# Performance work log

Measured on AMD Instinct MI355X. Metric: run time of the kernel, lower is better.

Reference implementation:

```python
import jax, jax.numpy as jnp
import numpy as np

STRIDES = (8, 16, 32, 64)
NUM_HEADS = 8
G = 4
P = 32
TAU_Z = 2.0
LVL_BASE = 3.0  # stride 8 == 2**3 maps to level 0


def decode_box(xyzr):
    scale = jnp.exp2(xyzr[..., 2:3])
    ratio = jnp.exp2(jnp.concatenate([-0.5 * xyzr[..., 3:4], 0.5 * xyzr[..., 3:4]], axis=-1))
    wh = scale * ratio
    xy = xyzr[..., 0:2]
    return jnp.concatenate([xy - 0.5 * wh, xy + 0.5 * wh], axis=-1)


def position_embedding(box, num_feats, temperature=10000.0):
    term = jnp.array([1000.0, 1000.0, 1.0, 1.0], dtype=box.dtype)
    token = box / term
    dim_t = jnp.arange(num_feats, dtype=jnp.float32)
    dim_t = temperature ** (2.0 * (dim_t // 2) / num_feats)
    pos = token[..., None] / dim_t  # B,N,4,F
    pos = jnp.stack([jnp.sin(pos[..., 0::2]), jnp.cos(pos[..., 1::2])], axis=4)
    B, N = box.shape[:2]
    return pos.reshape(B, N, -1)  # B,N,4*F


def bbox_iof(boxes):
    # boxes: B,N,4 x1y1x2y2; iof[b,i,j] = inter(i,j) / area(i)
    area = jnp.clip(boxes[..., 2] - boxes[..., 0], 0.0) * jnp.clip(boxes[..., 3] - boxes[..., 1], 0.0)
    lt = jnp.maximum(boxes[:, :, None, :2], boxes[:, None, :, :2])
    rb = jnp.minimum(boxes[:, :, None, 2:], boxes[:, None, :, 2:])
    wh = jnp.clip(rb - lt, 0.0)
    inter = wh[..., 0] * wh[..., 1]
    return inter / jnp.clip(area[:, :, None], 1e-7, None)


def bilinear_group_sample(feat, xy, stride):
    # feat: [B,C,H,W]; xy: [B,N,P,G,2] image coords -> [B,N,G,P,C//G]
    B, C, H, W = feat.shape
    _, N, Pn, Gn, _ = xy.shape
    Cg = C // Gn
    featg = feat.reshape(B, Gn, Cg, H * W).transpose(0, 1, 3, 2)  # B,G,HW,Cg
    px = xy[..., 0] / stride - 0.5  # grid_sample align_corners=False convention
    py = xy[..., 1] / stride - 0.5
    x0 = jnp.floor(px)
    y0 = jnp.floor(py)
    bi = jnp.arange(B)[:, None, None]
    gi = jnp.arange(Gn)[None, :, None]
    out = jnp.zeros((B, Gn, N * Pn, Cg), dtype=feat.dtype)
    for dx in (0.0, 1.0):
        for dy in (0.0, 1.0):
            xi = x0 + dx
            yi = y0 + dy
            wgt = (1.0 - jnp.abs(px - xi)) * (1.0 - jnp.abs(py - yi))
            valid = (xi >= 0) & (xi <= W - 1) & (yi >= 0) & (yi <= H - 1)
            wgt = wgt * valid  # zero padding outside
            xi_c = jnp.clip(xi, 0, W - 1).astype(jnp.int32)
            yi_c = jnp.clip(yi, 0, H - 1).astype(jnp.int32)
            idx = (yi_c * W + xi_c).transpose(0, 3, 1, 2).reshape(B, Gn, N * Pn)
            vals = featg[bi, gi, idx]  # B,G,N*P,Cg
            w = wgt.transpose(0, 3, 1, 2).reshape(B, Gn, N * Pn, 1)
            out = out + vals * w
    return out.reshape(B, Gn, N, Pn, Cg).transpose(0, 2, 1, 3, 4)


def layer_norm(x, g, b, eps=1e-5):
    mu = jnp.mean(x, axis=-1, keepdims=True)
    var = jnp.mean((x - mu) ** 2, axis=-1, keepdims=True)
    return (x - mu) * jax.lax.rsqrt(var + eps) * g + b


def _forward(feats, query_content, query_box, Wq, bq, Wk, bk, Wv, bv, Wo, bo,
             ln_g, ln_b, off_W, off_b, sc_W, sc_b, iof_tau):
    B, N, C = query_content.shape
    H = NUM_HEADS
    dh = C // H
    box_cxcy = query_box[..., :2]
    zc = query_box[..., 2:3]
    rc = query_box[..., 3:4]
    box_wh = jnp.exp2(zc) * jnp.exp2(jnp.concatenate([-0.5 * rc, 0.5 * rc], axis=-1))
    logscale = zc.reshape(B, N, 1, 1)

    # torch.no_grad() block -> stop_gradient
    rois = decode_box(query_box)
    iof = jnp.log(bbox_iof(jax.lax.stop_gradient(rois)) + 1e-7)  # B,N,N
    pe = jax.lax.stop_gradient(position_embedding(query_box, C // 4))  # B,N,C
    attn_bias = iof[:, None, :, :] * iof_tau.reshape(1, -1, 1, 1)  # B,H,N,N

    x = query_content + pe
    q = (x @ Wq.T + bq).reshape(B, N, H, dh)
    k = (x @ Wk.T + bk).reshape(B, N, H, dh)
    v = (x @ Wv.T + bv).reshape(B, N, H, dh)
    scores = jnp.einsum('bnhd,bmhd->bhnm', q, k) * (dh ** -0.5) + attn_bias
    attn = jax.nn.softmax(scores, axis=-1)
    ctx = jnp.einsum('bhnm,bmhd->bnhd', attn, v).reshape(B, N, C)
    qc = x + ctx @ Wo.T + bo  # mmcv MultiheadAttention adds identity (= query+pe)
    qc = layer_norm(qc, ln_g, ln_b)

    offset = (qc @ off_W.T + off_b).reshape(B, N, P, G, 2)
    scale_logit = (qc @ sc_W.T + sc_b).reshape(B, N, P, G)
    sample_xy = box_cxcy.reshape(B, N, 1, 1, 2) + offset * box_wh.reshape(B, N, 1, 1, 2)
    sample_z = scale_logit + logscale  # B,N,P,G
    lvl = sample_z - LVL_BASE
    levels = jnp.arange(len(STRIDES), dtype=jnp.float32)
    zw = jax.nn.softmax(-((lvl[..., None] - levels) ** 2) / TAU_Z, axis=-1)  # B,N,P,G,L
    zw_t = zw.transpose(0, 1, 3, 2, 4)  # B,N,G,P,L
    sample_feats = jnp.zeros(())
    for l, (fm, s) in enumerate(zip(feats, STRIDES)):
        sample_feats = sample_feats + bilinear_group_sample(fm, sample_xy, s) * zw_t[..., l:l + 1]
    return sample_feats, sample_xy, offset, sample_z, scale_logit, qc


def setup_inputs():
    key = jax.random.key(0)
    ks = jax.random.split(key, 20)
    B, N, C = 4, 500, 256
    feat0 = jax.random.normal(ks[0], (B, C, 128, 128), dtype=jnp.float32)
    feat1 = jax.random.normal(ks[1], (B, C, 64, 64), dtype=jnp.float32)
    feat2 = jax.random.normal(ks[2], (B, C, 32, 32), dtype=jnp.float32)
    feat3 = jax.random.normal(ks[3], (B, C, 16, 16), dtype=jnp.float32)
    query_content = jax.random.normal(ks[4], (B, N, C), dtype=jnp.float32)
    xy = jax.random.uniform(ks[5], (B, N, 2), minval=64.0, maxval=960.0)
    zz = jax.random.uniform(ks[6], (B, N, 1), minval=3.0, maxval=6.0)
    rr = jax.random.uniform(ks[7], (B, N, 1), minval=-1.0, maxval=1.0)
    query_box = jnp.concatenate([xy, zz, rr], axis=-1)
    sub_query_xy = jax.random.normal(ks[8], (B, N, P, G, 2), dtype=jnp.float32) * 0.1
    sub_query_z = jax.random.normal(ks[9], (B, N, P, G, 4), dtype=jnp.float32) * 0.1
    sub_query_vec = jax.random.normal(ks[10], (B, N, P, G, 64), dtype=jnp.float32) * 0.1
    imgs_whwh = jnp.full((B, N, 4), 1024.0, dtype=jnp.float32)
    w = lambda i, sh: jax.random.normal(ks[i], sh, dtype=jnp.float32) * 0.02
    return {
        'feat0': feat0, 'feat1': feat1, 'feat2': feat2, 'feat3': feat3,
        'query_content': query_content, 'query_box': query_box,
        'sub_query_xy': sub_query_xy, 'sub_query_z': sub_query_z,
        'sub_query_vec': sub_query_vec, 'imgs_whwh': imgs_whwh,
        'Wq': w(11, (C, C)), 'bq': jnp.zeros((C,), jnp.float32),
        'Wk': w(12, (C, C)), 'bk': jnp.zeros((C,), jnp.float32),
        'Wv': w(13, (C, C)), 'bv': jnp.zeros((C,), jnp.float32),
        'Wo': w(14, (C, C)), 'bo': jnp.zeros((C,), jnp.float32),
        'ln_g': jnp.ones((C,), jnp.float32), 'ln_b': jnp.zeros((C,), jnp.float32),
        'off_W': w(15, (2 * G * P, C)),
        'off_b': jax.random.uniform(ks[16], (2 * G * P,), minval=-0.5, maxval=0.5),
        'sc_W': w(17, (G * P, C)),
        'sc_b': jax.random.normal(ks[18], (G * P,), dtype=jnp.float32) * 0.1,
        'iof_tau': jax.random.uniform(ks[19], (NUM_HEADS,), minval=0.0, maxval=4.0),
    }


def reference(feat0, feat1, feat2, feat3, query_content, query_box, sub_query_xy,
              sub_query_z, sub_query_vec, imgs_whwh, Wq, bq, Wk, bk, Wv, bv, Wo, bo,
              ln_g, ln_b, off_W, off_b, sc_W, sc_b, iof_tau):
    sample_feats, sample_xy, offset, sample_z, scale_logit, qc = _forward(
        [feat0, feat1, feat2, feat3], query_content, query_box,
        Wq, bq, Wk, bk, Wv, bv, Wo, bo, ln_g, ln_b, off_W, off_b, sc_W, sc_b, iof_tau)
    return (sample_feats, sub_query_xy, sub_query_z, sub_query_vec, qc,
            sample_xy, offset, sample_z, scale_logit)
```

## Files before the change

### kernel.cpp

```cpp
#include <hip/hip_runtime.h>
#include <cstdint>
#include <cstddef>

#define B_ 4
#define N_ 500
#define C_ 256
#define NH_ 8
#define DH_ 32
#define P_ 32
#define G_ 4
#define CG_ 64
#define BN_ (B_*N_)

__constant__ const int LVL_W[4] = {128, 64, 32, 16};

static __device__ __forceinline__ unsigned short f2bf(float f) {
  union { float f; unsigned u; } v; v.f = f;
  unsigned r = v.u + 0x7FFF + ((v.u >> 16) & 1);
  return (unsigned short)(r >> 16);
}
static __device__ __forceinline__ float bf2f(unsigned u16shifted) {
  union { unsigned u; float f; } v; v.u = u16shifted;
  return v.f;
}

__global__ __launch_bounds__(256) void mega_kernel(
    const float* __restrict__ f0, const float* __restrict__ f1,
    const float* __restrict__ f2, const float* __restrict__ f3,
    unsigned short* __restrict__ t0, unsigned short* __restrict__ t1,
    unsigned short* __restrict__ t2, unsigned short* __restrict__ t3,
    const float* __restrict__ subxy, const float* __restrict__ subz,
    const float* __restrict__ subv,
    float* __restrict__ o_subxy, float* __restrict__ o_subz,
    float* __restrict__ o_subv, int tblocks) {
  __shared__ float tile[64][65];
  int blk = blockIdx.x;
  int t = threadIdx.x;
  if (blk < tblocks) {
    const float* src; unsigned short* dst; int npix, i;
    if (blk < 4096)      { src = f0; dst = t0; npix = 16384; i = blk; }
    else if (blk < 5120) { src = f1; dst = t1; npix = 4096;  i = blk - 4096; }
    else if (blk < 5376) { src = f2; dst = t2; npix = 1024;  i = blk - 5120; }
    else                 { src = f3; dst = t3; npix = 256;   i = blk - 5376; }
    int pb = npix >> 6;
    int p0 = (i % pb) * 64;
    int c0 = ((i / pb) & 3) * 64;
    int b  = i / (pb * 4);
    for (int k = 0; k < 16; k++) {
      int cl = k * 4 + (t >> 6);
      int pl = t & 63;
      tile[cl][pl] = src[((size_t)b * C_ + (c0 + cl)) * npix + (p0 + pl)];
    }
    __syncthreads();
    int cq = t & 15;
    for (int k = 0; k < 4; k++) {
      int pl = k * 16 + (t >> 4);
      ushort4 r;
      r.x = f2bf(tile[cq * 4 + 0][pl]);
      r.y = f2bf(tile[cq * 4 + 1][pl]);
      r.z = f2bf(tile[cq * 4 + 2][pl]);
      r.w = f2bf(tile[cq * 4 + 3][pl]);
      *(ushort4*)&dst[((size_t)b * npix + (p0 + pl)) * C_ + c0 + cq * 4] = r;
    }
  } else {
    int cb = blk - tblocks;
    const float4* s4; float4* d4;
    if (cb < 125)      { s4 = (const float4*)subxy + (size_t)cb * 1024;
                         d4 = (float4*)o_subxy + (size_t)cb * 1024; }
    else if (cb < 375) { s4 = (const float4*)subz + (size_t)(cb - 125) * 1024;
                         d4 = (float4*)o_subz + (size_t)(cb - 125) * 1024; }
    else               { s4 = (const float4*)subv + (size_t)(cb - 375) * 1024;
                         d4 = (float4*)o_subv + (size_t)(cb - 375) * 1024; }
    d4[t] = s4[t];
    d4[t + 256] = s4[t + 256];
    d4[t + 512] = s4[t + 512];
    d4[t + 768] = s4[t + 768];
  }
}

#define QKV_QI 8
__global__ __launch_bounds__(256) void qkv_prep_kernel(
    const float* __restrict__ qcontent, const float* __restrict__ qbox,
    const float* __restrict__ Wq, const float* __restrict__ bq,
    const float* __restrict__ Wk, const float* __restrict__ bk,
    const float* __restrict__ Wv, const float* __restrict__ bv,
    float* __restrict__ x, float* __restrict__ boxd,
    float* __restrict__ q, float* __restrict__ kT, float* __restrict__ vT) {
  __shared__ float xs[QKV_QI][C_];
  int blk = blockIdx.x;
  int t = threadIdx.x;
  int bn0 = blk * QKV_QI;
  int d = t >> 6;
  float tj = exp2f((float)((t >> 1) & 31) * 0.4152410f);
  float tmul = (d < 2) ? 0.001f : 1.0f;
  for (int i = 0; i < QKV_QI; i++) {
    float qv = qbox[(size_t)(bn0 + i) * 4 + d];
    float val = qv * tmul / tj;
    float pe = (t & 1) ? cosf(val) : sinf(val);
    float xv = qcontent[(size_t)(bn0 + i) * C_ + t] + pe;
    xs[i][t] = xv;
    x[(size_t)(bn0 + i) * C_ + t] = xv;
  }
  if (t < QKV_QI) {
    int bn = bn0 + t;
    const float* qb = qbox + (size_t)bn * 4;
    float cx = qb[0], cy = qb[1], z = qb[2], r = qb[3];
    float scale = exp2f(z);
    float w = scale * exp2f(-0.5f * r);
    float h = scale * exp2f(0.5f * r);
    float* bd = boxd + (size_t)bn * 12;
    float x1 = cx - 0.5f * w, y1 = cy - 0.5f * h, x2 = cx + 0.5f * w, y2 = cy + 0.5f * h;
    bd[0] = x1; bd[1] = y1; bd[2] = x2; bd[3] = y2;
    bd[4] = cx; bd[5] = cy; bd[6] = w; bd[7] = h; bd[8] = z;
    float area = fmaxf(x2 - x1, 0.f) * fmaxf(y2 - y1, 0.f);
    bd[9] = fmaxf(area, 1e-7f);
  }
  __syncthreads();
  float accq[QKV_QI], acck[QKV_QI], accv[QKV_QI];
  for (int i = 0; i < QKV_QI; i++) { accq[i] = 0.f; acck[i] = 0.f; accv[i] = 0.f; }
  const float4* wq4 = (const float4*)(Wq + (size_t)t * C_);
  const float4* wk4 = (const float4*)(Wk + (size_t)t * C_);
  const float4* wv4 = (const float4*)(Wv + (size_t)t * C_);
  for (int k4 = 0; k4 < C_ / 4; k4++) {
    float4 wq = wq4[k4], wk = wk4[k4], wv = wv4[k4];
    for (int i = 0; i < QKV_QI; i++) {
      float4 xv = *(const float4*)&xs[i][k4 * 4];
      accq[i] += xv.x * wq.x + xv.y * wq.y + xv.z * wq.z + xv.w * wq.w;
      acck[i] += xv.x * wk.x + xv.y * wk.y + xv.z * wk.z + xv.w * wk.w;
      accv[i] += xv.x * wv.x + xv.y * wv.y + xv.z * wv.z + xv.w * wv.w;
    }
  }
  for (int i = 0; i < QKV_QI; i++) {
    int bn = bn0 + i;
    int b = bn / N_;
    int n = bn % N_;
    q[(size_t)bn * C_ + t] = accq[i] + bq[t];
    kT[((size_t)b * C_ + t) * N_ + n] = acck[i] + bk[t];
    vT[((size_t)b * C_ + t) * N_ + n] = accv[i] + bv[t];
  }
}

__global__ __launch_bounds__(256) void score_kernel(
    const float* __restrict__ q, const float* __restrict__ kT,
    const float* __restrict__ boxd, const float* __restrict__ tau_p,
    float* __restrict__ S, float* __restrict__ Mpart) {
  int mp = blockIdx.x >> 1;
  int npar = blockIdx.x & 1;
  int h = blockIdx.y;
  int b = blockIdx.z;
  int w = threadIdx.x >> 6;
  int lane = threadIdx.x & 63;
  int m = mp * 64 + lane;
  int mc = min(m, N_ - 1);
  bool mok = m < N_;
  float tau = tau_p[h];
  const float scl = 0.17677669529663687f;

  float kreg[DH_];
  const float* kbase = kT + ((size_t)b * C_ + h * DH_) * N_ + mc;
#pragma unroll
  for (int d = 0; d < DH_; d++) kreg[d] = kbase[(size_t)d * N_];

  const float* bm = boxd + ((size_t)b * N_ + mc) * 12;
  float kx1 = bm[0], ky1 = bm[1], kx2 = bm[2], ky2 = bm[3];

  size_t srow_base = ((size_t)(b * NH_ + h)) * N_;
  for (int n = npar * 4 + w; n < N_; n += 8) {
    const float* qn = q + ((size_t)b * N_ + n) * C_ + h * DH_;
    float4 q0 = *(const float4*)&qn[0];
    float4 q1 = *(const float4*)&qn[4];
    float4 q2 = *(const float4*)&qn[8];
    float4 q3 = *(const float4*)&qn[12];
    float4 q4 = *(const float4*)&qn[16];
    float4 q5 = *(const float4*)&qn[20];
    float4 q6 = *(const float4*)&qn[24];
    float4 q7 = *(const float4*)&qn[28];
    float s0 = q0.x*kreg[0] + q0.y*kreg[1] + q0.z*kreg[2] + q0.w*kreg[3];
    float s1 = q1.x*kreg[4] + q1.y*kreg[5] + q1.z*kreg[6] + q1.w*kreg[7];
    float s2 = q2.x*kreg[8] + q2.y*kreg[9] + q2.z*kreg[10] + q2.w*kreg[11];
    float s3 = q3.x*kreg[12] + q3.y*kreg[13] + q3.z*kreg[14] + q3.w*kreg[15];
    s0 += q4.x*kreg[16] + q4.y*kreg[17] + q4.z*kreg[18] + q4.w*kreg[19];
    s1 += q5.x*kreg[20] + q5.y*kreg[21] + q5.z*kreg[22] + q5.w*kreg[23];
    s2 += q6.x*kreg[24] + q6.y*kreg[25] + q6.z*kreg[26] + q6.w*kreg[27];
    s3 += q7.x*kreg[28] + q7.y*kreg[29] + q7.z*kreg[30] + q7.w*kreg[31];
    float s = (s0 + s1) + (s2 + s3);

    const float* bn = boxd + ((size_t)b * N_ + n) * 12;
    float4 nb = *(const float4*)&bn[0];
    float inv_area = 1.0f / bn[9];
    float iw = fmaxf(fminf(nb.z, kx2) - fmaxf(nb.x, kx1), 0.f);
    float ih = fmaxf(fminf(nb.w, ky2) - fmaxf(nb.y, ky1), 0.f);
    float bias = logf(iw * ih * inv_area + 1e-7f);
    float sc = s * scl + bias * tau;

    if (mok) S[(srow_base + n) * 512 + m] = sc;
    float wm = mok ? sc : -1e30f;
#pragma unroll
    for (int off = 32; off >= 1; off >>= 1) wm = fmaxf(wm, __shfl_xor(wm, off, 64));
    if (lane == 0) Mpart[(srow_base + n) * 8 + mp] = wm;
  }
}

__global__ __launch_bounds__(256) void pv_kernel(
    const float* __restrict__ S, const float* __restrict__ Mpart,
    const float* __restrict__ vT, float* __restrict__ ctx) {
  int w = threadIdx.x >> 6;
  int lane = threadIdx.x & 63;
  int n0 = blockIdx.x * 4;
  int h = blockIdx.y * 4 + w;
  int b = blockIdx.z;
  size_t rb = ((size_t)(b * NH_ + h)) * N_;

  float mval = -1e30f;
  if (lane < 32) mval = Mpart[(rb + n0 + (lane >> 3)) * 8 + (lane & 7)];
  mval = fmaxf(mval, __shfl_xor(mval, 1, 64));
  mval = fmaxf(mval, __shfl_xor(mval, 2, 64));
  mval = fmaxf(mval, __shfl_xor(mval, 4, 64));
  float mx[4];
#pragma unroll
  for (int n = 0; n < 4; n++) mx[n] = __shfl(mval, n * 8, 64);

  float p[4][8];
  float inv[4];
#pragma unroll
  for (int n = 0; n < 4; n++) {
    const float* Srow = S + (rb + n0 + n) * 512;
    float sum = 0.f;
#pragma unroll
    for (int i = 0; i < 8; i++) {
      int m = lane + 64 * i;
      float sv = Srow[min(m, N_ - 1)];
      float e = (m < N_) ? __expf(sv - mx[n]) : 0.f;
      p[n][i] = e;
      sum += e;
    }
#pragma unroll
    for (int off = 32; off >= 1; off >>= 1) sum += __shfl_xor(sum, off, 64);
    inv[n] = 1.0f / sum;
  }

  const float* vbase = vT + ((size_t)b * C_ + h * DH_) * N_;
  float keep0 = 0.f, keep1 = 0.f, keep2 = 0.f, keep3 = 0.f;
  for (int cc = 0; cc < DH_; cc++) {
    const float* vrow = vbase + (size_t)cc * N_;
    float a0 = 0.f, a1 = 0.f, a2 = 0.f, a3 = 0.f;
#pragma unroll
    for (int i = 0; i < 8; i++) {
      int m = lane + 64 * i;
      float vv = vrow[min(m, N_ - 1)];
      a0 += p[0][i] * vv;
      a1 += p[1][i] * vv;
      a2 += p[2][i] * vv;
      a3 += p[3][i] * vv;
    }
#pragma unroll
    for (int off = 32; off >= 1; off >>= 1) {
      a0 += __shfl_xor(a0, off, 64);
      a1 += __shfl_xor(a1, off, 64);
      a2 += __shfl_xor(a2, off, 64);
      a3 += __shfl_xor(a3, off, 64);
    }
    bool sel = (lane & 31) == cc;
    keep0 = sel ? a0 : keep0;
    keep1 = sel ? a1 : keep1;
    keep2 = sel ? a2 : keep2;
    keep3 = sel ? a3 : keep3;
  }
  int c = lane & 31;
  size_t obase = ((size_t)b * N_ + n0) * C_ + h * DH_ + c;
  if (lane < 32) {
    ctx[obase + 0 * C_] = keep0 * inv[0];
    ctx[obase + 2 * C_] = keep2 * inv[2];
  } else {
    ctx[obase + 1 * C_] = keep1 * inv[1];
    ctx[obase + 3 * C_] = keep3 * inv[3];
  }
}

#define PQI 4
__global__ __launch_bounds__(256) void projln_head_kernel(
    const float* __restrict__ ctx, const float* __restrict__ x,
    const float* __restrict__ Wo, const float* __restrict__ bo,
    const float* __restrict__ ln_g, const float* __restrict__ ln_b,
    const float* __restrict__ boxd,
    const float* __restrict__ offW, const float* __restrict__ offb,
    const float* __restrict__ scW, const float* __restrict__ scb,
    float* __restrict__ qc_out,
    float* __restrict__ out_offset, float* __restrict__ out_sxy,
    float* __restrict__ out_sz, float* __restrict__ out_sl,
    float* __restrict__ zw_ws) {
  __shared__ float cs[PQI][C_];
  __shared__ float qs[PQI][C_];
  __shared__ float redbuf[PQI][8];
  int blk = blockIdx.x;
  int t = threadIdx.x;
  int bn0 = blk * PQI;
  for (int i = 0; i < PQI; i++) cs[i][t] = ctx[(size_t)(bn0 + i) * C_ + t];
  __syncthreads();
  float acc[PQI] = {0.f, 0.f, 0.f, 0.f};
  {
    const float4* w4 = (const float4*)(Wo + (size_t)t * C_);
    for (int k4 = 0; k4 < C_ / 4; k4++) {
      float4 w = w4[k4];
      for (int i = 0; i < PQI; i++) {
        float4 cv = *(const float4*)&cs[i][k4 * 4];
        acc[i] += cv.x * w.x + cv.y * w.y + cv.z * w.z + cv.w * w.w;
      }
    }
  }
  float y[PQI];
  int wave = t >> 6, lane = t & 63;
  for (int i = 0; i < PQI; i++) {
    y[i] = x[(size_t)(bn0 + i) * C_ + t] + acc[i] + bo[t];
    float s1 = y[i], s2 = y[i] * y[i];
#pragma unroll
    for (int off = 32; off >= 1; off >>= 1) {
      s1 += __shfl_xor(s1, off, 64);
      s2 += __shfl_xor(s2, off, 64);
    }
    if (lane == 0) { redbuf[i][wave] = s1; redbuf[i][wave + 4] = s2; }
  }
  __syncthreads();
  for (int i = 0; i < PQI; i++) {
    float s1 = redbuf[i][0] + redbuf[i][1] + redbuf[i][2] + redbuf[i][3];
    float s2 = redbuf[i][4] + redbuf[i][5] + redbuf[i][6] + redbuf[i][7];
    float mu = s1 * (1.0f / C_);
    float var = s2 * (1.0f / C_) - mu * mu;
    float inv = rsqrtf(var + 1e-5f);
    float o = (y[i] - mu) * inv * ln_g[t] + ln_b[t];
    qs[i][t] = o;
    qc_out[(size_t)(bn0 + i) * C_ + t] = o;
  }
  __syncthreads();
  float ao[PQI] = {0.f, 0.f, 0.f, 0.f};
  {
    const float4* w4 = (const float4*)(offW + (size_t)t * C_);
    for (int k4 = 0; k4 < C_ / 4; k4++) {
      float4 w = w4[k4];
      for (int i = 0; i < PQI; i++) {
        float4 cv = *(const float4*)&qs[i][k4 * 4];
        ao[i] += cv.x * w.x + cv.y * w.y + cv.z * w.z + cv.w * w.w;
      }
    }
  }
  int xy = t & 1;
  for (int i = 0; i < PQI; i++) {
    int bn = bn0 + i;
    const float* bd = boxd + (size_t)bn * 12;
    float off = ao[i] + offb[t];
    float ctr = xy ? bd[5] : bd[4];
    float wh = xy ? bd[7] : bd[6];
    float sxy = ctr + off * wh;
    out_offset[(size_t)bn * 256 + t] = off;
    out_sxy[(size_t)bn * 256 + t] = sxy;
  }
  if (t < 128) {
    float as[PQI] = {0.f, 0.f, 0.f, 0.f};
    const float4* sw4 = (const float4*)(scW + (size_t)t * C_);
    for (int k4 = 0; k4 < C_ / 4; k4++) {
      float4 w = sw4[k4];
      for (int i = 0; i < PQI; i++) {
        float4 cv = *(const float4*)&qs[i][k4 * 4];
        as[i] += cv.x * w.x + cv.y * w.y + cv.z * w.z + cv.w * w.w;
      }
    }
    for (int i = 0; i < PQI; i++) {
      int bn = bn0 + i;
      const float* bd = boxd + (size_t)bn * 12;
      float sl = as[i] + scb[t];
      float sz = sl + bd[8];
      out_sl[(size_t)bn * 128 + t] = sl;
      out_sz[(size_t)bn * 128 + t] = sz;
      float lvl = sz - 3.0f;
      float d1 = lvl - 1.f, d2 = lvl - 2.f, d3 = lvl - 3.f;
      float e0 = __expf(-0.5f * lvl * lvl);
      float e1 = __expf(-0.5f * d1 * d1);
      float e2 = __expf(-0.5f * d2 * d2);
      float e3 = __expf(-0.5f * d3 * d3);
      float inv = 1.0f / (e0 + e1 + e2 + e3);
      float* zw = zw_ws + ((size_t)bn * 128 + t) * 4;
      zw[0] = e0 * inv; zw[1] = e1 * inv; zw[2] = e2 * inv; zw[3] = e3 * inv;
    }
  }
}

__global__ __launch_bounds__(256) void sample_kernel_v3(
    const unsigned short* __restrict__ f0, const unsigned short* __restrict__ f1,
    const unsigned short* __restrict__ f2, const unsigned short* __restrict__ f3,
    const float* __restrict__ sxy, const float* __restrict__ zw_ws,
    float* __restrict__ out) {
  int t = threadIdx.x;
  int wv = t >> 6;
  int lane = t & 63;
  int sub = lane >> 4;
  int c4 = lane & 15;
  int pt = blockIdx.x * 16 + wv * 4 + sub;
  int g = pt & 3;
  int p = (pt >> 2) & 31;
  int bn = pt >> 7;
  int b = bn / N_;

  float sx = sxy[(size_t)pt * 2];
  float sy = sxy[(size_t)pt * 2 + 1];
  const float* zw = zw_ws + (size_t)pt * 4;
  const unsigned short* feats[4] = {f0, f1, f2, f3};
  const float inv_stride[4] = {0.125f, 0.0625f, 0.03125f, 0.015625f};
  float4 acc = {0.f, 0.f, 0.f, 0.f};
#pragma unroll
  for (int l = 0; l < 4; l++) {
    float wl = zw[l];
    int W = LVL_W[l];
    float px = sx * inv_stride[l] - 0.5f;
    float py = sy * inv_stride[l] - 0.5f;
    float x0f = floorf(px), y0f = floorf(py);
    float fx = px - x0f, fy = py - y0f;
    int x0 = (int)x0f, y0 = (int)y0f;
    const unsigned short* fb = feats[l] + (size_t)b * W * W * C_ + g * CG_ + c4 * 4;
#pragma unroll
    for (int dy = 0; dy < 2; dy++) {
#pragma unroll
      for (int dx = 0; dx < 2; dx++) {
        int xi = x0 + dx, yi = y0 + dy;
        float valid = (xi >= 0 && xi < W && yi >= 0 && yi < W) ? 1.f : 0.f;
        int xc = min(max(xi, 0), W - 1);
        int yc = min(max(yi, 0), W - 1);
        float wgt = (dx ? fx : 1.f - fx) * (dy ? fy : 1.f - fy) * valid * wl;
        uint2 u = *(const uint2*)&fb[((size_t)yc * W + xc) * C_];
        acc.x += wgt * bf2f(u.x << 16);
        acc.y += wgt * bf2f(u.x & 0xFFFF0000u);
        acc.z += wgt * bf2f(u.y << 16);
        acc.w += wgt * bf2f(u.y & 0xFFFF0000u);
      }
    }
  }
  *(float4*)&out[(size_t)bn * 8192 + g * 2048 + p * 64 + c4 * 4] = acc;
}

__global__ __launch_bounds__(256) void sample_kernel_native(
    const float* __restrict__ f0, const float* __restrict__ f1,
    const float* __restrict__ f2, const float* __restrict__ f3,
    const float* __restrict__ sxy, const float* __restrict__ zw_ws,
    float* __restrict__ out) {
  int t = threadIdx.x;
  int wv = t >> 6;
  int lane = t & 63;
  int pt = blockIdx.x * 4 + wv;
  int g = pt & 3;
  int p = (pt >> 2) & 31;
  int bn = pt >> 7;
  int b = bn / N_;
  float sx = sxy[(size_t)pt * 2];
  float sy = sxy[(size_t)pt * 2 + 1];
  const float* zw = zw_ws + (size_t)pt * 4;
  const float* feats[4] = {f0, f1, f2, f3};
  const float inv_stride[4] = {0.125f, 0.0625f, 0.03125f, 0.015625f};
  float acc = 0.f;
#pragma unroll
  for (int l = 0; l < 4; l++) {
    float wl = zw[l];
    int W = LVL_W[l];
    float px = sx * inv_stride[l] - 0.5f;
    float py = sy * inv_stride[l] - 0.5f;
    float x0f = floorf(px), y0f = floorf(py);
    float fx = px - x0f, fy = py - y0f;
    int x0 = (int)x0f, y0 = (int)y0f;
#pragma unroll
    for (int dy = 0; dy < 2; dy++) {
#pragma unroll
      for (int dx = 0; dx < 2; dx++) {
        int xi = x0 + dx, yi = y0 + dy;
        if (xi >= 0 && xi < W && yi >= 0 && yi < W) {
          float wgt = (dx ? fx : 1.f - fx) * (dy ? fy : 1.f - fy);
          float v = feats[l][(((size_t)b * C_ + g * CG_ + lane) * W + yi) * W + xi];
          acc += wgt * wl * v;
        }
      }
    }
  }
  out[(size_t)bn * 8192 + g * 2048 + p * 64 + lane] = acc;
}

extern "C" void kernel_launch(void* const* d_in, const int* in_sizes, int n_in,
                              void* d_out, int out_size, void* d_ws, size_t ws_size,
                              hipStream_t stream) {
  (void)in_sizes; (void)n_in; (void)out_size;
  const float* feat[4] = {(const float*)d_in[0], (const float*)d_in[1],
                          (const float*)d_in[2], (const float*)d_in[3]};
  const float* query_content = (const float*)d_in[4];
  const float* query_box = (const float*)d_in[5];
  const float* Wq = (const float*)d_in[10]; const float* bq = (const float*)d_in[11];
  const float* Wk = (const float*)d_in[12]; const float* bk = (const float*)d_in[13];
  const float* Wv = (const float*)d_in[14]; const float* bv = (const float*)d_in[15];
  const float* Wo = (const float*)d_in[16]; const float* bo = (const float*)d_in[17];
  const float* ln_g = (const float*)d_in[18]; const float* ln_b = (const float*)d_in[19];
  const float* offW = (const float*)d_in[20]; const float* offb = (const float*)d_in[21];
  const float* scW = (const float*)d_in[22]; const float* scb = (const float*)d_in[23];
  const float* iof_tau = (const float*)d_in[24];

  float* out = (float*)d_out;
  float* ws = (float*)d_ws;

  const size_t O_FEATS = 0;
  const size_t O_SUBXY = 16384000;
  const size_t O_SUBZ = 16896000;
  const size_t O_SUBV = 17920000;
  const size_t O_QC = 34304000;
  const size_t O_SXY = 34816000;
  const size_t O_OFF = 35328000;
  const size_t O_SZ = 35840000;
  const size_t O_SL = 36096000;

  float* S = out + O_FEATS;
  float* Mpart = out + O_FEATS + 8192000;

  const size_t o_x = 0;
  const size_t o_boxd = o_x + 512000;
  const size_t o_q = o_boxd + 24000;
  const size_t o_kT = o_q + 512000;
  const size_t o_vT = o_kT + 512000;
  const size_t o_ctx = o_vT + 512000;
  const size_t o_zw = o_ctx + 512000;
  const size_t o_ft = o_zw + 1024000;
  const size_t ft_sz[4] = {16777216, 4194304, 1048576, 262144};
  const size_t ft_total = ft_sz[0] + ft_sz[1] + ft_sz[2] + ft_sz[3];
  const size_t need_T = o_ft * sizeof(float) + ft_total * sizeof(unsigned short);
  const bool useT = ws_size >= need_T;

  unsigned short* ftu = (unsigned short*)(ws + o_ft);
  unsigned short* ftb[4] = {ftu,
                            ftu + ft_sz[0],
                            ftu + ft_sz[0] + ft_sz[1],
                            ftu + ft_sz[0] + ft_sz[1] + ft_sz[2]};

  const int tblocks = useT ? 5440 : 0;
  const int cblocks = 4375;
  mega_kernel<<<tblocks + cblocks, 256, 0, stream>>>(
      feat[0], feat[1], feat[2], feat[3],
      ftb[0], ftb[1], ftb[2], ftb[3],
      (const float*)d_in[6], (const float*)d_in[7], (const float*)d_in[8],
      out + O_SUBXY, out + O_SUBZ, out + O_SUBV, tblocks);

  qkv_prep_kernel<<<BN_ / QKV_QI, 256, 0, stream>>>(
      query_content, query_box, Wq, bq, Wk, bk, Wv, bv,
      ws + o_x, ws + o_boxd, ws + o_q, ws + o_kT, ws + o_vT);

  {
    dim3 ga(16, NH_, B_);
    score_kernel<<<ga, 256, 0, stream>>>(ws + o_q, ws + o_kT, ws + o_boxd, iof_tau, S, Mpart);
    dim3 gb(N_ / 4, 2, B_);
    pv_kernel<<<gb, 256, 0, stream>>>(S, Mpart, ws + o_vT, ws + o_ctx);
  }

  projln_head_kernel<<<BN_ / PQI, 256, 0, stream>>>(
      ws + o_ctx, ws + o_x, Wo, bo, ln_g, ln_b, ws + o_boxd,
      offW, offb, scW, scb,
      out + O_QC, out + O_OFF, out + O_SXY, out + O_SZ, out + O_SL,
      ws + o_zw);

  const int npoints = BN_ * P_ * G_;
  if (useT) {
    sample_kernel_v3<<<npoints / 16, 256, 0, stream>>>(
        ftb[0], ftb[1], ftb[2], ftb[3],
        out + O_SXY, ws + o_zw, out + O_FEATS);
  } else {
    sample_kernel_native<<<npoints / 4, 256, 0, stream>>>(
        feat[0], feat[1], feat[2], feat[3],
        out + O_SXY, ws + o_zw, out + O_FEATS);
  }
}
```

Before: 302.7 us.

## Fold QKV projection into transpose/copy mega kernel and vectorize transpose loads

Merges the QKV/positional-embedding prep kernel into the existing mega kernel as an extra range of blocks, so the projection runs alongside the feature transpose and copy work and one launch is removed. Shared memory is now a union of the transpose tile and the QKV staging buffer. The transpose read path switches from scalar loads to float4 loads along pixels. The merged kernel may need more registers and lower occupancy because the QKV branch keeps 24 accumulators per thread.

```diff
diff --git a/kernel.cpp b/kernel.cpp
--- a/kernel.cpp
+++ b/kernel.cpp
@@ -11,6 +11,7 @@
 #define G_ 4
 #define CG_ 64
 #define BN_ (B_*N_)
+#define QKV_QI 8
 
 __constant__ const int LVL_W[4] = {128, 64, 32, 16};
 
@@ -32,8 +33,18 @@
     const float* __restrict__ subxy, const float* __restrict__ subz,
     const float* __restrict__ subv,
     float* __restrict__ o_subxy, float* __restrict__ o_subz,
-    float* __restrict__ o_subv, int tblocks) {
-  __shared__ float tile[64][65];
+    float* __restrict__ o_subv,
+    const float* __restrict__ qcontent, const float* __restrict__ qbox,
+    const float* __restrict__ Wq, const float* __restrict__ bq,
+    const float* __restrict__ Wk, const float* __restrict__ bk,
+    const float* __restrict__ Wv, const float* __restrict__ bv,
+    float* __restrict__ x, float* __restrict__ boxd,
+    float* __restrict__ q, float* __restrict__ kT, float* __restrict__ vT,
+    int tblocks, int cblocks) {
+  __shared__ union {
+    float tile[64][65];
+    float xs[QKV_QI][C_];
+  } sm;
   int blk = blockIdx.x;
   int t = threadIdx.x;
   if (blk < tblocks) {
@@ -46,23 +57,30 @@
     int p0 = (i % pb) * 64;
     int c0 = ((i / pb) & 3) * 64;
     int b  = i / (pb * 4);
-    for (int k = 0; k < 16; k++) {
-      int cl = k * 4 + (t >> 6);
-      int pl = t & 63;
-      tile[cl][pl] = src[((size_t)b * C_ + (c0 + cl)) * npix + (p0 + pl)];
+    int col4 = t & 15;
+    int rsub = t >> 4;
+#pragma unroll
+    for (int k = 0; k < 4; k++) {
+      int row = k * 16 + rsub;
+      float4 v = *(const float4*)&src[((size_t)b * C_ + (c0 + row)) * npix + p0 + col4 * 4];
+      sm.tile[row][col4 * 4 + 0] = v.x;
+      sm.tile[row][col4 * 4 + 1] = v.y;
+      sm.tile[row][col4 * 4 + 2] = v.z;
+      sm.tile[row][col4 * 4 + 3] = v.w;
     }
     __syncthreads();
     int cq = t & 15;
+#pragma unroll
     for (int k = 0; k < 4; k++) {
       int pl = k * 16 + (t >> 4);
       ushort4 r;
-      r.x = f2bf(tile[cq * 4 + 0][pl]);
-      r.y = f2bf(tile[cq * 4 + 1][pl]);
-      r.z = f2bf(tile[cq * 4 + 2][pl]);
-      r.w = f2bf(tile[cq * 4 + 3][pl]);
+      r.x = f2bf(sm.tile[cq * 4 + 0][pl]);
+      r.y = f2bf(sm.tile[cq * 4 + 1][pl]);
+      r.z = f2bf(sm.tile[cq * 4 + 2][pl]);
+      r.w = f2bf(sm.tile[cq * 4 + 3][pl]);
       *(ushort4*)&dst[((size_t)b * npix + (p0 + pl)) * C_ + c0 + cq * 4] = r;
     }
-  } else {
+  } else if (blk < tblocks + cblocks) {
     int cb = blk - tblocks;
     const float4* s4; float4* d4;
     if (cb < 125)      { s4 = (const float4*)subxy + (size_t)cb * 1024;
@@ -75,68 +93,56 @@
     d4[t + 256] = s4[t + 256];
     d4[t + 512] = s4[t + 512];
     d4[t + 768] = s4[t + 768];
-  }
-}
-
-#define QKV_QI 8
-__global__ __launch_bounds__(256) void qkv_prep_kernel(
-    const float* __restrict__ qcontent, const float* __restrict__ qbox,
-    const float* __restrict__ Wq, const float* __restrict__ bq,
-    const float* __restrict__ Wk, const float* __restrict__ bk,
-    const float* __restrict__ Wv, const float* __restrict__ bv,
-    float* __restrict__ x, float* __restrict__ boxd,
-    float* __restrict__ q, float* __restrict__ kT, float* __restrict__ vT) {
-  __shared__ float xs[QKV_QI][C_];
-  int blk = blockIdx.x;
-  int t = threadIdx.x;
-  int bn0 = blk * QKV_QI;
-  int d = t >> 6;
-  float tj = exp2f((float)((t >> 1) & 31) * 0.4152410f);
-  float tmul = (d < 2) ? 0.001f : 1.0f;
-  for (int i = 0; i < QKV_QI; i++) {
-    float qv = qbox[(size_t)(bn0 + i) * 4 + d];
-    float val = qv * tmul / tj;
-    float pe = (t & 1) ? cosf(val) : sinf(val);
-    float xv = qcontent[(size_t)(bn0 + i) * C_ + t] + pe;
-    xs[i][t] = xv;
-    x[(size_t)(bn0 + i) * C_ + t] = xv;
-  }
-  if (t < QKV_QI) {
-    int bn = bn0 + t;
-    const float* qb = qbox + (size_t)bn * 4;
-    float cx = qb[0], cy = qb[1], z = qb[2], r = qb[3];
-    float scale = exp2f(z);
-    float w = scale * exp2f(-0.5f * r);
-    float h = scale * exp2f(0.5f * r);
-    float* bd = boxd + (size_t)bn * 12;
-    float x1 = cx - 0.5f * w, y1 = cy - 0.5f * h, x2 = cx + 0.5f * w, y2 = cy + 0.5f * h;
-    bd[0] = x1; bd[1] = y1; bd[2] = x2; bd[3] = y2;
-    bd[4] = cx; bd[5] = cy; bd[6] = w; bd[7] = h; bd[8] = z;
-    float area = fmaxf(x2 - x1, 0.f) * fmaxf(y2 - y1, 0.f);
-    bd[9] = fmaxf(area, 1e-7f);
-  }
-  __syncthreads();
-  float accq[QKV_QI], acck[QKV_QI], accv[QKV_QI];
-  for (int i = 0; i < QKV_QI; i++) { accq[i] = 0.f; acck[i] = 0.f; accv[i] = 0.f; }
-  const float4* wq4 = (const float4*)(Wq + (size_t)t * C_);
-  const float4* wk4 = (const float4*)(Wk + (size_t)t * C_);
-  const float4* wv4 = (const float4*)(Wv + (size_t)t * C_);
-  for (int k4 = 0; k4 < C_ / 4; k4++) {
-    float4 wq = wq4[k4], wk = wk4[k4], wv = wv4[k4];
+  } else {
+    int bn0 = (blk - tblocks - cblocks) * QKV_QI;
+    int d = t >> 6;
+    float tj = exp2f((float)((t >> 1) & 31) * 0.4152410f);
+    float tmul = (d < 2) ? 0.001f : 1.0f;
     for (int i = 0; i < QKV_QI; i++) {
-      float4 xv = *(const float4*)&xs[i][k4 * 4];
-      accq[i] += xv.x * wq.x + xv.y * wq.y + xv.z * wq.z + xv.w * wq.w;
-      acck[i] += xv.x * wk.x + xv.y * wk.y + xv.z * wk.z + xv.w * wk.w;
-      accv[i] += xv.x * wv.x + xv.y * wv.y + xv.z * wv.z + xv.w * wv.w;
-    }
-  }
-  for (int i = 0; i < QKV_QI; i++) {
-    int bn = bn0 + i;
-    int b = bn / N_;
-    int n = bn % N_;
-    q[(size_t)bn * C_ + t] = accq[i] + bq[t];
-    kT[((size_t)b * C_ + t) * N_ + n] = acck[i] + bk[t];
-    vT[((size_t)b * C_ + t) * N_ + n] = accv[i] + bv[t];
+      float qv = qbox[(size_t)(bn0 + i) * 4 + d];
+      float val = qv * tmul / tj;
+      float pe = (t & 1) ? cosf(val) : sinf(val);
+      float xv = qcontent[(size_t)(bn0 + i) * C_ + t] + pe;
+      sm.xs[i][t] = xv;
+      x[(size_t)(bn0 + i) * C_ + t] = xv;
+    }
+    if (t < QKV_QI) {
+      int bn = bn0 + t;
+      const float* qb = qbox + (size_t)bn * 4;
+      float cx = qb[0], cy = qb[1], z = qb[2], r = qb[3];
+      float scale = exp2f(z);
+      float w = scale * exp2f(-0.5f * r);
+      float h = scale * exp2f(0.5f * r);
+      float* bd = boxd + (size_t)bn * 12;
+      float x1 = cx - 0.5f * w, y1 = cy - 0.5f * h, x2 = cx + 0.5f * w, y2 = cy + 0.5f * h;
+      bd[0] = x1; bd[1] = y1; bd[2] = x2; bd[3] = y2;
+      bd[4] = cx; bd[5] = cy; bd[6] = w; bd[7] = h; bd[8] = z;
+      float area = fmaxf(x2 - x1, 0.f) * fmaxf(y2 - y1, 0.f);
+      bd[9] = fmaxf(area, 1e-7f);
+    }
+    __syncthreads();
+    float accq[QKV_QI], acck[QKV_QI], accv[QKV_QI];
+    for (int i = 0; i < QKV_QI; i++) { accq[i] = 0.f; acck[i] = 0.f; accv[i] = 0.f; }
+    const float4* wq4 = (const float4*)(Wq + (size_t)t * C_);
+    const float4* wk4 = (const float4*)(Wk + (size_t)t * C_);
+    const float4* wv4 = (const float4*)(Wv + (size_t)t * C_);
+    for (int k4 = 0; k4 < C_ / 4; k4++) {
+      float4 wq = wq4[k4], wk = wk4[k4], wv = wv4[k4];
+      for (int i = 0; i < QKV_QI; i++) {
+        float4 xv = *(const float4*)&sm.xs[i][k4 * 4];
+        accq[i] += xv.x * wq.x + xv.y * wq.y + xv.z * wq.z + xv.w * wq.w;
+        acck[i] += xv.x * wk.x + xv.y * wk.y + xv.z * wk.z + xv.w * wk.w;
+        accv[i] += xv.x * wv.x + xv.y * wv.y + xv.z * wv.z + xv.w * wv.w;
+      }
+    }
+    for (int i = 0; i < QKV_QI; i++) {
+      int bn = bn0 + i;
+      int b = bn / N_;
+      int n = bn % N_;
+      q[(size_t)bn * C_ + t] = accq[i] + bq[t];
+      kT[((size_t)b * C_ + t) * N_ + n] = acck[i] + bk[t];
+      vT[((size_t)b * C_ + t) * N_ + n] = accv[i] + bv[t];
+    }
   }
 }
 
@@ -534,15 +540,15 @@
 
   const int tblocks = useT ? 5440 : 0;
   const int cblocks = 4375;
-  mega_kernel<<<tblocks + cblocks, 256, 0, stream>>>(
+  const int qblocks = BN_ / QKV_QI;
+  mega_kernel<<<tblocks + cblocks + qblocks, 256, 0, stream>>>(
       feat[0], feat[1], feat[2], feat[3],
       ftb[0], ftb[1], ftb[2], ftb[3],
       (const float*)d_in[6], (const float*)d_in[7], (const float*)d_in[8],
-      out + O_SUBXY, out + O_SUBZ, out + O_SUBV, tblocks);
-
-  qkv_prep_kernel<<<BN_ / QKV_QI, 256, 0, stream>>>(
+      out + O_SUBXY, out + O_SUBZ, out + O_SUBV,
       query_content, query_box, Wq, bq, Wk, bk, Wv, bv,
-      ws + o_x, ws + o_boxd, ws + o_q, ws + o_kT, ws + o_vT);
+      ws + o_x, ws + o_boxd, ws + o_q, ws + o_kT, ws + o_vT,
+      tblocks, cblocks);
 
   {
     dim3 ga(16, NH_, B_);
```

New measurement: 319.8 us. 5.6% more time.
